# Performance work log

Measured on AMD Instinct MI355X. Metric: run time of the kernel, lower is better.

The kernel has to match this reference:

```python
import jax, jax.numpy as jnp
import numpy as np

D_MODEL = 768
N_HEADS = 12
D_K = D_MODEL // N_HEADS
NEG_INF = -1e9


def setup_inputs() -> dict:
    key = jax.random.key(0)
    ks = jax.random.split(key, 7)
    B, S = 4, 2048
    x = jax.random.normal(ks[0], (B, S, D_MODEL), dtype=jnp.float32)
    # causal mask, broadcastable to [B, H, S, S]
    mask = jnp.tril(jnp.ones((S, S), dtype=bool))[None, None, :, :]
    scale = 1.0 / np.sqrt(D_MODEL)
    Wq = jax.random.normal(ks[1], (D_MODEL, D_MODEL), dtype=jnp.float32) * scale
    bq = jnp.zeros((D_MODEL,), dtype=jnp.float32)
    Wk = jax.random.normal(ks[2], (D_MODEL, D_MODEL), dtype=jnp.float32) * scale
    bk = jnp.zeros((D_MODEL,), dtype=jnp.float32)
    Wv = jax.random.normal(ks[3], (D_MODEL, D_MODEL), dtype=jnp.float32) * scale
    bv = jnp.zeros((D_MODEL,), dtype=jnp.float32)
    return {"x": x, "mask": mask, "Wq": Wq, "bq": bq, "Wk": Wk, "bk": bk, "Wv": Wv, "bv": bv}


def reference(x, mask, Wq, bq, Wk, bk, Wv, bv):
    B, S, _ = x.shape
    # projections (torch Linear: y = x @ W.T + b)
    q = (x @ Wq.T + bq).reshape(B, S, N_HEADS, D_K)
    k = (x @ Wk.T + bk).reshape(B, S, N_HEADS, D_K)
    v = (x @ Wv.T + bv).reshape(B, S, N_HEADS, D_K)
    # scores: [B, H, S, S]
    scores = jnp.einsum("bqhd,bkhd->bhqk", q, k) / jnp.sqrt(jnp.float32(D_K))
    scores = jnp.where(mask, scores, NEG_INF)
    probs = jax.nn.softmax(scores, axis=-1)
    # attention: [B, H, S, D_K] -> [B, S, d_model]
    attn = jnp.einsum("bhqk,bkhd->bqhd", probs, v).reshape(B, S, D_MODEL)
    return attn
```

## Files before the change

### kernel.cpp

```cpp
#include <hip/hip_runtime.h>
#include <math.h>


#define S_LEN 2048
#define BATCH 4
#define HEADS 12
#define DM 768
#define DK 64
#define BH (BATCH*HEADS)
#define MROWS (BATCH*S_LEN)
#define QSCALE 0.1803368801111244f

typedef __attribute__((ext_vector_type(8))) short short8;
typedef __attribute__((ext_vector_type(4))) float floatx4;
typedef __attribute__((ext_vector_type(16))) float floatx16;
typedef __attribute__((ext_vector_type(4))) unsigned int uintx4;
typedef __attribute__((address_space(3))) unsigned char lds_byte;
typedef __attribute__((address_space(1))) const unsigned char glob_byte;

__device__ __forceinline__ unsigned short f2bf(float f) {
  union { float f; unsigned int u; } a; a.f = f;
  unsigned int u = a.u;
  return (unsigned short)((u + 0x7fffu + ((u >> 16) & 1u)) >> 16);
}

__global__ __launch_bounds__(256) void cast_all(
    const float* __restrict__ x,
    const float* __restrict__ w0, const float* __restrict__ w1,
    const float* __restrict__ w2,
    unsigned short* __restrict__ xb, unsigned short* __restrict__ wb) {
  const int NX = MROWS * DM, NW = DM * DM;
  int i = (blockIdx.x * 256 + threadIdx.x) * 4;
  const float* src; unsigned short* dst; int off;
  if (i < NX) { src = x; dst = xb; off = i; }
  else {
    int kk = i - NX; int s = kk / NW; off = kk - s * NW;
    src = (s == 0) ? w0 : (s == 1) ? w1 : w2;
    dst = wb + (size_t)s * NW;
  }
  float4 v = *(const float4*)(src + off);
  ushort4 o;
  o.x = f2bf(v.x); o.y = f2bf(v.y); o.z = f2bf(v.z); o.w = f2bf(v.w);
  *(ushort4*)(dst + off) = o;
}

__global__ __launch_bounds__(256) void qkv_gemm(
    const unsigned short* __restrict__ xb,
    const unsigned short* __restrict__ wb,
    const float* __restrict__ bq, const float* __restrict__ bk,
    const float* __restrict__ bv,
    unsigned short* __restrict__ qo,
    unsigned short* __restrict__ ko,
    unsigned short* __restrict__ vto) {
  __shared__ unsigned short a_lds[2 * 128 * 32];
  __shared__ unsigned short b_lds[2 * 128 * 32];
  const int mat = blockIdx.z;
  const int tid = threadIdx.x;
  const int wave = tid >> 6, lane = tid & 63, quad = lane >> 4, ln = lane & 15;
  const int wm = wave & 1, wn = wave >> 1;
  const int m_blk = blockIdx.x * 128, n_blk = blockIdx.y * 128;
  const unsigned short* w = wb + (size_t)mat * DM * DM;
  const int srow_i[2] = { (0 * 256 + wave * 64 + lane) >> 2,
                          (1 * 256 + wave * 64 + lane) >> 2 };
  const int sq = (lane & 3) * 8;

  const floatx4 fz = {0.f, 0.f, 0.f, 0.f};
  floatx4 acc[4][4];
#pragma unroll
  for (int mg = 0; mg < 4; mg++)
#pragma unroll
    for (int c = 0; c < 4; c++) acc[mg][c] = fz;

  for (int k0 = 0; k0 < DM; k0 += 64) {
#pragma unroll
    for (int p = 0; p < 2; p++)
#pragma unroll
      for (int i = 0; i < 2; i++) {
        const int cbase = i * 256 + wave * 64;
        const int row = srow_i[i];
        __builtin_amdgcn_global_load_lds(
            (glob_byte*)(xb + (size_t)(m_blk + row) * DM + k0 + p * 32 + sq),
            (lds_byte*)(a_lds + p * 4096 + cbase * 8), 16, 0, 0);
        __builtin_amdgcn_global_load_lds(
            (glob_byte*)(w + (size_t)(n_blk + row) * DM + k0 + p * 32 + sq),
            (lds_byte*)(b_lds + p * 4096 + cbase * 8), 16, 0, 0);
      }
    __syncthreads();

    short8 af[4][2], bf[4][2];
#pragma unroll
    for (int mg = 0; mg < 4; mg++)
#pragma unroll
      for (int p = 0; p < 2; p++)
        af[mg][p] = *(const short8*)(a_lds + p * 4096 + (wm * 64 + mg * 16 + ln) * 32 + quad * 8);
#pragma unroll
    for (int c = 0; c < 4; c++)
#pragma unroll
      for (int p = 0; p < 2; p++)
        bf[c][p] = *(const short8*)(b_lds + p * 4096 + (wn * 64 + c * 16 + ln) * 32 + quad * 8);
#pragma unroll
    for (int mg = 0; mg < 4; mg++)
#pragma unroll
      for (int c = 0; c < 4; c++) {
        acc[mg][c] = __builtin_amdgcn_mfma_f32_16x16x32_bf16(af[mg][0], bf[c][0], acc[mg][c], 0, 0, 0);
        acc[mg][c] = __builtin_amdgcn_mfma_f32_16x16x32_bf16(af[mg][1], bf[c][1], acc[mg][c], 0, 0, 0);
      }
    __syncthreads();
  }

  const float* bias = (mat == 0) ? bq : (mat == 1) ? bk : bv;
  const float oscale = (mat == 0) ? QSCALE : 1.0f;
  const int m_base = m_blk + wm * 64, n_base = n_blk + wn * 64;
#pragma unroll
  for (int mg = 0; mg < 4; mg++)
#pragma unroll
    for (int c = 0; c < 4; c++) {
      int gn = n_base + c * 16 + ln;
      int hd = gn >> 6, d = gn & 63;
      float bias_v = bias[gn] * oscale;
      int gm0 = m_base + mg * 16 + quad * 4;
      int bb = gm0 >> 11, s0 = gm0 & (S_LEN - 1);
      if (mat == 2) {
        ushort4 pk;
        pk.x = f2bf(acc[mg][c][0] + bias_v);
        pk.y = f2bf(acc[mg][c][1] + bias_v);
        pk.z = f2bf(acc[mg][c][2] + bias_v);
        pk.w = f2bf(acc[mg][c][3] + bias_v);
        *(ushort4*)(vto + (((size_t)(bb * HEADS + hd)) * DK + d) * S_LEN + s0) = pk;
      } else {
        unsigned short* dst = (mat == 0 ? qo : ko) +
            (((size_t)(bb * HEADS + hd)) * S_LEN + s0) * DK + d;
#pragma unroll
        for (int r = 0; r < 4; r++)
          dst[(size_t)r * DK] = f2bf(acc[mg][c][r] * oscale + bias_v);
      }
    }
}

__global__ __launch_bounds__(256) void flash_attn(
    const unsigned short* __restrict__ q,
    const unsigned short* __restrict__ k,
    const unsigned short* __restrict__ vt,
    float* __restrict__ out) {
  __shared__ unsigned short k_lds[3][64 * 64];
  __shared__ unsigned short v_lds[3][64 * 64];
  const int id0 = blockIdx.x;
  const int rr = id0 >> 8, jj = id0 & 255;
  const int g = (rr == 0) ? jj : (rr == 1) ? (511 - jj) : (512 + jj);
  const int bh = g % BH;
  const int qt = (S_LEN / 128 - 1) - (g / BH);
  const int q0 = qt * 128;
  const int tid = threadIdx.x;
  const int wave = tid >> 6, lane = tid & 63;
  const int l31 = lane & 31, hi = lane >> 5;
  const unsigned short* qp = q + (size_t)bh * S_LEN * DK;
  const unsigned char* kpb = (const unsigned char*)(k  + (size_t)bh * S_LEN * DK);
  const unsigned char* vpb = (const unsigned char*)(vt + (size_t)bh * DK * S_LEN);
  const int qr_base = q0 + wave * 32;

  const floatx16 fz16 = {0.f,0.f,0.f,0.f,0.f,0.f,0.f,0.f,
                         0.f,0.f,0.f,0.f,0.f,0.f,0.f,0.f};

  short8 ones;
#pragma unroll
  for (int j = 0; j < 8; j++) ones[j] = (short)0x3F80;

  short8 aq[4];
#pragma unroll
  for (int ks = 0; ks < 4; ks++)
    aq[ks] = *(const short8*)(qp + (size_t)(qr_base + l31) * DK + ks * 16 + hi * 8);

  floatx16 o0 = fz16, o1 = fz16, lacc = fz16;

  const int sc0 = tid, sc1 = 256 + tid;
  const int sr[2]  = { sc0 >> 3, sc1 >> 3 };
  const int ssb[2] = { ((sc0 & 7) * 16) ^ ((sr[0] & 7) << 4),
                       ((sc1 & 7) * 16) ^ ((sr[1] & 7) << 4) };

  auto stage = [&](unsigned short* kd, unsigned short* vd, int k0) {
#pragma unroll
    for (int i = 0; i < 2; i++) {
      const int cbase = i * 256 + wave * 64;
      __builtin_amdgcn_global_load_lds(
          (glob_byte*)(kpb + (size_t)(k0 + sr[i]) * 128 + ssb[i]),
          (lds_byte*)(kd + cbase * 8), 16, 0, 0);
      __builtin_amdgcn_global_load_lds(
          (glob_byte*)(vpb + (size_t)sr[i] * (S_LEN * 2) + k0 * 2 + ssb[i]),
          (lds_byte*)(vd + cbase * 8), 16, 0, 0);
    }
  };

  const int xr = (l31 & 7) << 4;

  auto body = [&](int k0, const unsigned short* kbp, const unsigned short* vbp) {
    const unsigned char* kb = (const unsigned char*)kbp;
    const unsigned char* vb = (const unsigned char*)vbp;
    const bool domask = (k0 + 63 > qr_base);
#pragma unroll
    for (int kg = 0; kg < 2; kg++) {
      floatx16 sc = fz16;
      __builtin_amdgcn_s_setprio(1);
#pragma unroll
      for (int ks = 0; ks < 4; ks++) {
        short8 kf = *(const short8*)(kb + (kg * 32 + l31) * 128 + ((ks * 32 + hi * 16) ^ xr));
        sc = __builtin_amdgcn_mfma_f32_32x32x16_bf16(kf, aq[ks], sc, 0, 0, 0);
      }
      __builtin_amdgcn_s_setprio(0);
      float pv[16];
      const int qr = qr_base + l31;
#pragma unroll
      for (int r = 0; r < 16; r++) {
        float e2 = exp2f(sc[r]);
        if (domask) {
          int key = k0 + kg * 32 + (r & 3) + 8 * (r >> 2) + 4 * hi;
          e2 = (key <= qr) ? e2 : 0.f;
        }
        pv[r] = e2;
      }
      unsigned int dw[4][2];
#pragma unroll
      for (int b = 0; b < 4; b++)
#pragma unroll
        for (int c = 0; c < 2; c++)
          asm("v_cvt_pk_bf16_f32 %0, %1, %2"
              : "=v"(dw[b][c]) : "v"(pv[4 * b + 2 * c]), "v"(pv[4 * b + 2 * c + 1]));
#pragma unroll
      for (int ks2 = 0; ks2 < 2; ks2++) {
        unsigned int a0 = dw[2 * ks2][0], a1 = dw[2 * ks2][1];
        unsigned int b0 = dw[2 * ks2 + 1][0], b1 = dw[2 * ks2 + 1][1];
        asm("v_permlane32_swap_b32 %0, %1" : "+v"(a0), "+v"(b0));
        asm("v_permlane32_swap_b32 %0, %1" : "+v"(a1), "+v"(b1));
        union { uintx4 u; short8 s; } ap;
        ap.u = (uintx4){a0, a1, b0, b1};
        short8 vf0 = *(const short8*)(vb + (0 * 32 + l31) * 128 + ((kg * 64 + ks2 * 32 + hi * 16) ^ xr));
        short8 vf1 = *(const short8*)(vb + (1 * 32 + l31) * 128 + ((kg * 64 + ks2 * 32 + hi * 16) ^ xr));
        __builtin_amdgcn_s_setprio(1);
        o0 = __builtin_amdgcn_mfma_f32_32x32x16_bf16(ap.s, vf0, o0, 0, 0, 0);
        o1 = __builtin_amdgcn_mfma_f32_32x32x16_bf16(ap.s, vf1, o1, 0, 0, 0);
        lacc = __builtin_amdgcn_mfma_f32_32x32x16_bf16(ap.s, ones, lacc, 0, 0, 0);
        __builtin_amdgcn_s_setprio(0);
      }
    }
  };

  const int nt = (q0 + 128) / 64;
  const int qmax = qr_base + 31;

  unsigned short *kA = &k_lds[0][0], *kB = &k_lds[1][0], *kC = &k_lds[2][0];
  unsigned short *vA = &v_lds[0][0], *vB = &v_lds[1][0], *vC = &v_lds[2][0];

  stage(kA, vA, 0);
  stage(kB, vB, 64);
  __syncthreads();

#pragma unroll 1
  for (int t = 0; t < nt; ++t) {
    if (t + 2 < nt) stage(kC, vC, (t + 2) * 64);
    if (t * 64 <= qmax) body(t * 64, kA, vA);
    if (t + 1 < nt) {
      if (t + 2 < nt) {
        asm volatile("s_waitcnt vmcnt(4)" ::: "memory");
      } else {
        asm volatile("s_waitcnt vmcnt(0)" ::: "memory");
      }
      __builtin_amdgcn_s_barrier();
      __builtin_amdgcn_sched_barrier(0);
    }
    unsigned short* tk = kA; kA = kB; kB = kC; kC = tk;
    unsigned short* tv = vA; vA = vB; vB = vC; vC = tv;
  }

  const int b = bh / HEADS, hd = bh % HEADS;
#pragma unroll
  for (int r = 0; r < 16; r++) {
    float inv = 1.f / lacc[r];
    int qrow = qr_base + (r & 3) + 8 * (r >> 2) + 4 * hi;
    float* orow = out + ((size_t)(b * S_LEN + qrow)) * DM + hd * DK;
    orow[l31]      = o0[r] * inv;
    orow[32 + l31] = o1[r] * inv;
  }
}

extern "C" void kernel_launch(void* const* d_in, const int* in_sizes, int n_in,
                              void* d_out, int out_size, void* d_ws, size_t ws_size,
                              hipStream_t stream) {
  const float* x  = (const float*)d_in[0];
  const float* Wq = (const float*)d_in[2];
  const float* bq = (const float*)d_in[3];
  const float* Wk = (const float*)d_in[4];
  const float* bk = (const float*)d_in[5];
  const float* Wv = (const float*)d_in[6];
  const float* bv = (const float*)d_in[7];
  float* out = (float*)d_out;

  const int NX = MROWS * DM;
  const int NW = DM * DM;
  const size_t NQK = (size_t)BH * S_LEN * DK;
  unsigned short* xb = (unsigned short*)d_ws;
  unsigned short* wb = xb + NX;
  unsigned short* qo = wb + 3 * NW;
  unsigned short* ko = qo + NQK;
  unsigned short* vt = ko + NQK;

  cast_all<<<(NX + 3 * NW) / 4 / 256, 256, 0, stream>>>(x, Wq, Wk, Wv, xb, wb);

  qkv_gemm<<<dim3(MROWS / 128, DM / 128, 3), 256, 0, stream>>>(
      xb, wb, bq, bk, bv, qo, ko, vt);

  flash_attn<<<dim3((S_LEN / 128) * BH), 256, 0, stream>>>(qo, ko, vt, out);
}
```

Before: 209.2 us.

## Software-pipeline QK of next tile with softmax and PV of current tile

After: 243.1 us. 1.16x slower.

```diff
diff --git a/kernel.cpp b/kernel.cpp
--- a/kernel.cpp
+++ b/kernel.cpp
@@ -137,13 +137,13 @@
     }
 }
 
-__global__ __launch_bounds__(256) void flash_attn(
+__global__ __launch_bounds__(256, 1) void flash_attn(
     const unsigned short* __restrict__ q,
     const unsigned short* __restrict__ k,
     const unsigned short* __restrict__ vt,
     float* __restrict__ out) {
-  __shared__ unsigned short k_lds[3][64 * 64];
-  __shared__ unsigned short v_lds[3][64 * 64];
+  __shared__ unsigned short k_lds[2][64 * 64];
+  __shared__ unsigned short v_lds[2][64 * 64];
   const int id0 = blockIdx.x;
   const int rr = id0 >> 8, jj = id0 & 255;
   const int g = (rr == 0) ? jj : (rr == 1) ? (511 - jj) : (512 + jj);
@@ -171,6 +171,7 @@
     aq[ks] = *(const short8*)(qp + (size_t)(qr_base + l31) * DK + ks * 16 + hi * 8);
 
   floatx16 o0 = fz16, o1 = fz16, lacc = fz16;
+  floatx16 scE[2], scO[2];
 
   const int sc0 = tid, sc1 = 256 + tid;
   const int sr[2]  = { sc0 >> 3, sc1 >> 3 };
@@ -192,25 +193,43 @@
 
   const int xr = (l31 & 7) << 4;
 
-  auto body = [&](int k0, const unsigned short* kbp, const unsigned short* vbp) {
+  auto qk = [&](const unsigned short* kbp, floatx16 (&sc)[2]) {
     const unsigned char* kb = (const unsigned char*)kbp;
-    const unsigned char* vb = (const unsigned char*)vbp;
-    const bool domask = (k0 + 63 > qr_base);
+    __builtin_amdgcn_s_setprio(1);
 #pragma unroll
     for (int kg = 0; kg < 2; kg++) {
-      floatx16 sc = fz16;
-      __builtin_amdgcn_s_setprio(1);
+      floatx16 s = fz16;
 #pragma unroll
       for (int ks = 0; ks < 4; ks++) {
         short8 kf = *(const short8*)(kb + (kg * 32 + l31) * 128 + ((ks * 32 + hi * 16) ^ xr));
-        sc = __builtin_amdgcn_mfma_f32_32x32x16_bf16(kf, aq[ks], sc, 0, 0, 0);
-      }
-      __builtin_amdgcn_s_setprio(0);
+        s = __builtin_amdgcn_mfma_f32_32x32x16_bf16(kf, aq[ks], s, 0, 0, 0);
+      }
+      sc[kg] = s;
+    }
+    __builtin_amdgcn_s_setprio(0);
+  };
+
+  auto vload = [&](const unsigned short* vbp, short8 (&vf)[2][2][2]) {
+    const unsigned char* vb = (const unsigned char*)vbp;
+#pragma unroll
+    for (int dg = 0; dg < 2; dg++)
+#pragma unroll
+      for (int kg = 0; kg < 2; kg++)
+#pragma unroll
+        for (int ks2 = 0; ks2 < 2; ks2++)
+          vf[dg][kg][ks2] = *(const short8*)(vb + (dg * 32 + l31) * 128 +
+                                             ((kg * 64 + ks2 * 32 + hi * 16) ^ xr));
+  };
+
+  auto sv = [&](int k0, const floatx16 (&sc)[2], const short8 (&vf)[2][2][2]) {
+    const bool domask = (k0 + 63 > qr_base);
+    const int qr = qr_base + l31;
+#pragma unroll
+    for (int kg = 0; kg < 2; kg++) {
       float pv[16];
-      const int qr = qr_base + l31;
 #pragma unroll
       for (int r = 0; r < 16; r++) {
-        float e2 = exp2f(sc[r]);
+        float e2 = exp2f(sc[kg][r]);
         if (domask) {
           int key = k0 + kg * 32 + (r & 3) + 8 * (r >> 2) + 4 * hi;
           e2 = (key <= qr) ? e2 : 0.f;
@@ -232,42 +251,38 @@
         asm("v_permlane32_swap_b32 %0, %1" : "+v"(a1), "+v"(b1));
         union { uintx4 u; short8 s; } ap;
         ap.u = (uintx4){a0, a1, b0, b1};
-        short8 vf0 = *(const short8*)(vb + (0 * 32 + l31) * 128 + ((kg * 64 + ks2 * 32 + hi * 16) ^ xr));
-        short8 vf1 = *(const short8*)(vb + (1 * 32 + l31) * 128 + ((kg * 64 + ks2 * 32 + hi * 16) ^ xr));
         __builtin_amdgcn_s_setprio(1);
-        o0 = __builtin_amdgcn_mfma_f32_32x32x16_bf16(ap.s, vf0, o0, 0, 0, 0);
-        o1 = __builtin_amdgcn_mfma_f32_32x32x16_bf16(ap.s, vf1, o1, 0, 0, 0);
+        o0 = __builtin_amdgcn_mfma_f32_32x32x16_bf16(ap.s, vf[0][kg][ks2], o0, 0, 0, 0);
+        o1 = __builtin_amdgcn_mfma_f32_32x32x16_bf16(ap.s, vf[1][kg][ks2], o1, 0, 0, 0);
         lacc = __builtin_amdgcn_mfma_f32_32x32x16_bf16(ap.s, ones, lacc, 0, 0, 0);
         __builtin_amdgcn_s_setprio(0);
       }
     }
   };
 
+  unsigned short* const kb0 = &k_lds[0][0]; unsigned short* const vb0 = &v_lds[0][0];
+  unsigned short* const kb1 = &k_lds[1][0]; unsigned short* const vb1 = &v_lds[1][0];
   const int nt = (q0 + 128) / 64;
   const int qmax = qr_base + 31;
 
-  unsigned short *kA = &k_lds[0][0], *kB = &k_lds[1][0], *kC = &k_lds[2][0];
-  unsigned short *vA = &v_lds[0][0], *vB = &v_lds[1][0], *vC = &v_lds[2][0];
-
-  stage(kA, vA, 0);
-  stage(kB, vB, 64);
+  stage(kb0, vb0, 0);
+  stage(kb1, vb1, 64);
   __syncthreads();
-
+  qk(kb0, scE);
+
+  short8 vf[2][2][2];
 #pragma unroll 1
-  for (int t = 0; t < nt; ++t) {
-    if (t + 2 < nt) stage(kC, vC, (t + 2) * 64);
-    if (t * 64 <= qmax) body(t * 64, kA, vA);
-    if (t + 1 < nt) {
-      if (t + 2 < nt) {
-        asm volatile("s_waitcnt vmcnt(4)" ::: "memory");
-      } else {
-        asm volatile("s_waitcnt vmcnt(0)" ::: "memory");
-      }
-      __builtin_amdgcn_s_barrier();
-      __builtin_amdgcn_sched_barrier(0);
-    }
-    unsigned short* tk = kA; kA = kB; kB = kC; kC = tk;
-    unsigned short* tv = vA; vA = vB; vB = vC; vC = tv;
+  for (int t = 0; t < nt; t += 2) {
+    vload(vb0, vf);
+    __syncthreads();
+    if (t + 2 < nt) stage(kb0, vb0, (t + 2) * 64);
+    if ((t + 1) * 64 <= qmax) qk(kb1, scO);
+    if (t * 64 <= qmax) sv(t * 64, scE, vf);
+    vload(vb1, vf);
+    __syncthreads();
+    if (t + 3 < nt) stage(kb1, vb1, (t + 3) * 64);
+    if (t + 2 < nt && (t + 2) * 64 <= qmax) qk(kb0, scE);
+    if ((t + 1) * 64 <= qmax) sv((t + 1) * 64, scO, vf);
   }
 
   const int b = bh / HEADS, hd = bh % HEADS;
```
